# Kernel optimization log

Hardware: AMD Instinct MI355X
Metric: run time of the kernel (lower is better)

## Reference

```python
import jax, jax.numpy as jnp
import numpy as np

B, S, INP, HID = 64, 2048, 512, 512

def setup_inputs() -> dict:
    key = jax.random.key(0)
    ks = jax.random.split(key, 8)
    inp = jax.random.normal(ks[0], (B, INP), dtype=jnp.float32)
    context = jax.random.normal(ks[1], (B, S, INP), dtype=jnp.float32)
    mask = jax.random.randint(ks[2], (B, S), 0, 2) == 1  # True = masked out
    lim_l = 1.0 / np.sqrt(INP)
    Wl = jax.random.uniform(ks[3], (HID, INP), minval=-lim_l, maxval=lim_l, dtype=jnp.float32)
    bl = jax.random.uniform(ks[4], (HID,), minval=-lim_l, maxval=lim_l, dtype=jnp.float32)
    Wc = jax.random.uniform(ks[5], (HID, INP), minval=-lim_l, maxval=lim_l, dtype=jnp.float32)  # Conv1d k=1 weight squeezed
    bc = jax.random.uniform(ks[6], (HID,), minval=-lim_l, maxval=lim_l, dtype=jnp.float32)
    V = jax.random.uniform(ks[7], (HID,), minval=-1.0, maxval=1.0, dtype=jnp.float32)
    return {"inp": inp, "context": context, "mask": mask,
            "Wl": Wl, "bl": bl, "Wc": Wc, "bc": bc, "V": V}

def reference(inp, context, mask, Wl, bl, Wc, bc, V):
    # hid: [B, HID], broadcast over S
    hid = inp @ Wl.T + bl
    # 1x1 Conv1d over permuted context == per-position linear: [B, HID, S]
    ctx = jnp.einsum('bsi,hi->bhs', context, Wc) + bc[None, :, None]
    # additive attention scores: [B, S]
    att = jnp.einsum('h,bhs->bs', V, jnp.tanh(hid[:, :, None] + ctx))
    att = jnp.where(mask, -jnp.inf, att)
    alpha = jax.nn.softmax(att, axis=1)
    # context vector: [B, HID]
    hidden_state = jnp.einsum('bhs,bs->bh', ctx, alpha)
    return (hidden_state, alpha)
```

## Files before the change

### kernel.cpp

```cpp
#include <hip/hip_runtime.h>
#include <hip/hip_bf16.h>
#include <cstdint>
#include <cstddef>

#define B_   64
#define S_   2048
#define INP_ 512
#define HID_ 512

typedef float          floatx4  __attribute__((ext_vector_type(4)));
typedef __bf16         bf16x8   __attribute__((ext_vector_type(8)));
typedef unsigned short ushortx8 __attribute__((ext_vector_type(8)));
typedef unsigned short ushortx4 __attribute__((ext_vector_type(4)));

__device__ __forceinline__ unsigned short f2bf(float f) {
  unsigned u = __float_as_uint(f);
  u += 0x7FFFu + ((u >> 16) & 1u);
  return (unsigned short)(u >> 16);
}
__device__ __forceinline__ float bf2f(unsigned short h) {
  return __uint_as_float(((unsigned)h) << 16);
}
__device__ __forceinline__ float fast_tanh(float x) {
  float u = __builtin_amdgcn_exp2f(x * 2.88539008177792681472f);
  return 1.0f - 2.0f * __builtin_amdgcn_rcpf(u + 1.0f);
}

__global__ void hid_kernel(const float* __restrict__ inp, const float* __restrict__ Wl,
                           const float* __restrict__ bl, float* __restrict__ hid)
{
  __shared__ float ism[512];
  const int b = blockIdx.x, t = threadIdx.x;
  ism[t]       = inp[b * 512 + t];
  ism[t + 256] = inp[b * 512 + 256 + t];
  __syncthreads();
  #pragma unroll
  for (int hh = 0; hh < 2; ++hh) {
    int h = t + hh * 256;
    const float4* wr = (const float4*)(Wl + (size_t)h * 512);
    float4 sv = {0.f, 0.f, 0.f, 0.f};
    for (int i = 0; i < 128; ++i) {
      float4 wv = wr[i];
      float4 iv = *(const float4*)(&ism[i * 4]);
      sv.x += wv.x * iv.x; sv.y += wv.y * iv.y;
      sv.z += wv.z * iv.z; sv.w += wv.w * iv.w;
    }
    hid[b * 512 + h] = bl[h] + sv.x + sv.y + sv.z + sv.w;
  }
}

__global__ void pack_wc_kernel(const float* __restrict__ Wc, unsigned short* __restrict__ pk)
{
  int g = blockIdx.x * 256 + threadIdx.x;
  int l = g & 63, ks = (g >> 6) & 15, m16 = g >> 10;
  int row = m16 * 16 + (l & 15);
  int kb  = ks * 32 + (l >> 4) * 8;
  const float4* s = (const float4*)(Wc + (size_t)row * 512 + kb);
  float4 a = s[0], c = s[1];
  ushortx8 o = { f2bf(a.x), f2bf(a.y), f2bf(a.z), f2bf(a.w),
                 f2bf(c.x), f2bf(c.y), f2bf(c.z), f2bf(c.w) };
  *(ushortx8*)(pk + (size_t)g * 8) = o;
}

template<int MODE>
__global__ __launch_bounds__(256, 2) void ctx_gemm_kernel(
    const float* __restrict__ context, const unsigned short* __restrict__ Wc_pk,
    const float* __restrict__ hid, const float* __restrict__ bc,
    const float* __restrict__ V,
    unsigned short* __restrict__ ctx_out, float* __restrict__ att,
    const float* __restrict__ alpha, float* __restrict__ hidden)
{
  __shared__ alignas(16) unsigned short bsm[64 * 128];
  __shared__ float hid_sm[512];
  __shared__ float V_sm[512];
  __shared__ float bc_sm[512];
  __shared__ float att_sm[64];
  __shared__ float alpha_sm[64];

  const int b    = blockIdx.y;
  const int s0   = blockIdx.x * 64;
  const int t    = threadIdx.x;
  const int lane = t & 63;
  const int w    = t >> 6;
  const int quad = lane >> 4;
  const int l15  = lane & 15;

  for (int i = t; i < 512; i += 256) {
    hid_sm[i] = hid[b * 512 + i];
    V_sm[i]   = V[i];
    bc_sm[i]  = bc[i];
  }
  if (t < 64) {
    att_sm[t] = 0.0f;
    if (MODE == 2) alpha_sm[t] = alpha[b * S_ + s0 + t];
  }

  floatx4 acc[8][4];
  #pragma unroll
  for (int m = 0; m < 8; ++m)
    #pragma unroll
    for (int n = 0; n < 4; ++n) { floatx4 z = {0.f,0.f,0.f,0.f}; acc[m][n] = z; }

  const unsigned short* apBase = Wc_pk + (size_t)(w * 8) * 8192 + lane * 8;
  const float* src = context + ((size_t)b * S_ + s0) * INP_;

  for (int phase = 0; phase < 4; ++phase) {
    __syncthreads();
    #pragma unroll
    for (int i = 0; i < 8; ++i) {
      int id  = t + i * 256;
      int row = id >> 5;
      int c4  = id & 31;
      float4 f = *(const float4*)(src + (size_t)row * INP_ + phase * 128 + c4 * 4);
      int chunk = c4 >> 1, half = c4 & 1;
      int sw = chunk ^ (row & 7);
      ushortx4 hv = { f2bf(f.x), f2bf(f.y), f2bf(f.z), f2bf(f.w) };
      *(ushortx4*)(&bsm[row * 128 + sw * 8 + half * 4]) = hv;
    }
    __syncthreads();
    #pragma unroll
    for (int ksl = 0; ksl < 4; ++ksl) {
      const int ksg = phase * 4 + ksl;
      bf16x8 af[8];
      #pragma unroll
      for (int m = 0; m < 8; ++m)
        af[m] = *(const bf16x8*)(apBase + (size_t)m * 8192 + ksg * 512);
      bf16x8 bfr[4];
      #pragma unroll
      for (int n = 0; n < 4; ++n) {
        int row = n * 16 + l15;
        int c   = ksl * 4 + quad;
        bfr[n] = *(const bf16x8*)(&bsm[row * 128 + ((c ^ (row & 7)) * 8)]);
      }
      #pragma unroll
      for (int m = 0; m < 8; ++m)
        #pragma unroll
        for (int n = 0; n < 4; ++n)
          acc[m][n] = __builtin_amdgcn_mfma_f32_16x16x32_bf16(af[m], bfr[n], acc[m][n], 0, 0, 0);
    }
  }

  if (MODE == 0 || MODE == 1) {
    float attacc[4] = {0.f, 0.f, 0.f, 0.f};
    #pragma unroll
    for (int m = 0; m < 8; ++m) {
      int hb = w * 128 + m * 16 + quad * 4;
      #pragma unroll
      for (int r = 0; r < 4; ++r) {
        int h = hb + r;
        float bcv = bc_sm[h], hv = hid_sm[h], vv = V_sm[h];
        #pragma unroll
        for (int n = 0; n < 4; ++n) {
          float val = acc[m][n][r] + bcv;
          if (MODE == 0)
            ctx_out[((size_t)b * HID_ + h) * S_ + s0 + n * 16 + l15] = f2bf(val);
          attacc[n] += vv * fast_tanh(hv + val);
        }
      }
    }
    #pragma unroll
    for (int n = 0; n < 4; ++n) {
      float v = attacc[n];
      v += __shfl_xor(v, 16);
      v += __shfl_xor(v, 32);
      if (lane < 16) atomicAdd(&att_sm[n * 16 + l15], v);
    }
    __syncthreads();
    if (t < 64) att[b * S_ + s0 + t] = att_sm[t];
  } else {
    #pragma unroll
    for (int m = 0; m < 8; ++m) {
      int hb = w * 128 + m * 16 + quad * 4;
      #pragma unroll
      for (int r = 0; r < 4; ++r) {
        int h = hb + r;
        float bcv = bc_sm[h];
        float hacc = 0.0f;
        #pragma unroll
        for (int n = 0; n < 4; ++n)
          hacc += (acc[m][n][r] + bcv) * alpha_sm[n * 16 + l15];
        hacc += __shfl_xor(hacc, 1);
        hacc += __shfl_xor(hacc, 2);
        hacc += __shfl_xor(hacc, 4);
        hacc += __shfl_xor(hacc, 8);
        if (l15 == 0) atomicAdd(&hidden[b * HID_ + h], hacc);
      }
    }
  }
}

__global__ void softmax_kernel(const void* __restrict__ mask,
                               const float* __restrict__ att,
                               float* __restrict__ alpha)
{
  __shared__ int flags;
  __shared__ float red[8];
  const int b = blockIdx.x, t = threadIdx.x;
  const int lane = t & 63, w = t >> 6;
  if (t == 0) flags = 0;
  __syncthreads();
  int f = 0;
  const unsigned* mw = (const unsigned*)mask;
  for (int i = t; i < 512; i += 256) {
    unsigned v = mw[i];
    if (v > 1u) f |= 1;
    if (v != 0u && v != 0x3f800000u) f |= 2;
  }
  if (f) atomicOr(&flags, f);
  __syncthreads();
  const int fl = flags;
  const int mode = ((fl & 1) == 0) ? 0 : (((fl & 2) == 0) ? 1 : 2);

  float v[8]; bool msk[8];
  float vmax = -1e30f;
  #pragma unroll
  for (int i = 0; i < 8; ++i) {
    int idx = i * 256 + t;
    bool m;
    if (mode == 0)      m = ((const int*)mask)[b * S_ + idx] != 0;
    else if (mode == 1) m = ((const float*)mask)[b * S_ + idx] != 0.0f;
    else                m = ((const unsigned char*)mask)[b * S_ + idx] != 0;
    msk[i] = m;
    v[i] = att[b * S_ + idx];
    if (!m) vmax = fmaxf(vmax, v[i]);
  }
  #pragma unroll
  for (int off = 32; off; off >>= 1) vmax = fmaxf(vmax, __shfl_xor(vmax, off));
  if (lane == 0) red[w] = vmax;
  __syncthreads();
  vmax = fmaxf(fmaxf(red[0], red[1]), fmaxf(red[2], red[3]));

  float e[8], s = 0.0f;
  #pragma unroll
  for (int i = 0; i < 8; ++i) {
    e[i] = msk[i] ? 0.0f : __builtin_amdgcn_exp2f((v[i] - vmax) * 1.4426950408889634f);
    s += e[i];
  }
  #pragma unroll
  for (int off = 32; off; off >>= 1) s += __shfl_xor(s, off);
  if (lane == 0) red[4 + w] = s;
  __syncthreads();
  s = red[4] + red[5] + red[6] + red[7];
  float rinv = 1.0f / s;
  #pragma unroll
  for (int i = 0; i < 8; ++i)
    alpha[b * S_ + i * 256 + t] = e[i] * rinv;
}

__global__ void hidden_kernel(const unsigned short* __restrict__ ctx,
                              const float* __restrict__ alpha,
                              float* __restrict__ hidden)
{
  const int b = blockIdx.y;
  const int w = threadIdx.x >> 6, lane = threadIdx.x & 63;
  const int h = blockIdx.x * 4 + w;
  const unsigned short* cp = ctx + ((size_t)b * HID_ + h) * S_;
  const float* ap = alpha + (size_t)b * S_;
  float acc = 0.0f;
  #pragma unroll
  for (int it = 0; it < 4; ++it) {
    int s = it * 512 + lane * 8;
    ushortx8 cv = *(const ushortx8*)(cp + s);
    float4 a0 = *(const float4*)(ap + s);
    float4 a1 = *(const float4*)(ap + s + 4);
    acc += bf2f(cv[0]) * a0.x + bf2f(cv[1]) * a0.y + bf2f(cv[2]) * a0.z + bf2f(cv[3]) * a0.w
         + bf2f(cv[4]) * a1.x + bf2f(cv[5]) * a1.y + bf2f(cv[6]) * a1.z + bf2f(cv[7]) * a1.w;
  }
  #pragma unroll
  for (int off = 32; off; off >>= 1) acc += __shfl_xor(acc, off);
  if (lane == 0) hidden[b * HID_ + h] = acc;
}

extern "C" void kernel_launch(void* const* d_in, const int* in_sizes, int n_in,
                              void* d_out, int out_size, void* d_ws, size_t ws_size,
                              hipStream_t stream)
{
  const float* inp     = (const float*)d_in[0];
  const float* context = (const float*)d_in[1];
  const void*  mask    = d_in[2];
  const float* Wl      = (const float*)d_in[3];
  const float* bl      = (const float*)d_in[4];
  const float* Wc      = (const float*)d_in[5];
  const float* bc      = (const float*)d_in[6];
  const float* V       = (const float*)d_in[7];

  float* hidden = (float*)d_out;
  float* alpha  = (float*)d_out + B_ * HID_;

  char* ws = (char*)d_ws;
  const size_t CTX_BYTES = (size_t)B_ * HID_ * S_ * 2;
  const size_t HIDW_BYTES = (size_t)B_ * HID_ * 4;
  const size_t ATT_BYTES  = (size_t)B_ * S_ * 4;
  const size_t PK_BYTES   = (size_t)HID_ * INP_ * 2;
  const bool big = ws_size >= CTX_BYTES + HIDW_BYTES + ATT_BYTES + PK_BYTES;

  if (big) {
    unsigned short* ctx_bf = (unsigned short*)ws;
    float* hid_ws          = (float*)(ws + CTX_BYTES);
    float* att_ws          = (float*)(ws + CTX_BYTES + HIDW_BYTES);
    unsigned short* pk     = (unsigned short*)(ws + CTX_BYTES + HIDW_BYTES + ATT_BYTES);

    hid_kernel<<<B_, 256, 0, stream>>>(inp, Wl, bl, hid_ws);
    pack_wc_kernel<<<128, 256, 0, stream>>>(Wc, pk);
    ctx_gemm_kernel<0><<<dim3(S_ / 64, B_), 256, 0, stream>>>(
        context, pk, hid_ws, bc, V, ctx_bf, att_ws, nullptr, nullptr);
    softmax_kernel<<<B_, 256, 0, stream>>>(mask, att_ws, alpha);
    hidden_kernel<<<dim3(HID_ / 4, B_), 256, 0, stream>>>(ctx_bf, alpha, hidden);
  } else {
    float* hid_ws      = (float*)ws;
    float* att_ws      = (float*)(ws + HIDW_BYTES);
    unsigned short* pk = (unsigned short*)(ws + HIDW_BYTES + ATT_BYTES);

    hid_kernel<<<B_, 256, 0, stream>>>(inp, Wl, bl, hid_ws);
    pack_wc_kernel<<<128, 256, 0, stream>>>(Wc, pk);
    ctx_gemm_kernel<1><<<dim3(S_ / 64, B_), 256, 0, stream>>>(
        context, pk, hid_ws, bc, V, nullptr, att_ws, nullptr, nullptr);
    softmax_kernel<<<B_, 256, 0, stream>>>(mask, att_ws, alpha);
    hipMemsetAsync(hidden, 0, HIDW_BYTES, stream);
    ctx_gemm_kernel<2><<<dim3(S_ / 64, B_), 256, 0, stream>>>(
        context, pk, hid_ws, bc, V, nullptr, nullptr, alpha, hidden);
  }
}
```

Measured before the change: 519.9 us.

## Compute hidden state as Wc·(alpha-weighted context) instead of storing ctx

Uses linearity: since alpha sums to one, hidden = Wc·(Σ alpha·context) + bc. The bf16 ctx tensor is no longer written or read back. A new ctxbar kernel reduces context by alpha and a row-GEMV applies Wc and bc. The main GEMM now loads context into LDS with global_load_lds and converts fp32 to bf16 when building the MFMA fragments; hid and V are read from global in the epilogue. This costs a second full read of the fp32 context in exchange for dropping the large ctx write and read; the hid GEMV is also rewritten as a wave-per-row dot product.

```diff
diff --git a/kernel.cpp b/kernel.cpp
--- a/kernel.cpp
+++ b/kernel.cpp
@@ -11,42 +11,31 @@
 typedef float          floatx4  __attribute__((ext_vector_type(4)));
 typedef __bf16         bf16x8   __attribute__((ext_vector_type(8)));
 typedef unsigned short ushortx8 __attribute__((ext_vector_type(8)));
-typedef unsigned short ushortx4 __attribute__((ext_vector_type(4)));
 
 __device__ __forceinline__ unsigned short f2bf(float f) {
   unsigned u = __float_as_uint(f);
   u += 0x7FFFu + ((u >> 16) & 1u);
   return (unsigned short)(u >> 16);
 }
-__device__ __forceinline__ float bf2f(unsigned short h) {
-  return __uint_as_float(((unsigned)h) << 16);
-}
 __device__ __forceinline__ float fast_tanh(float x) {
   float u = __builtin_amdgcn_exp2f(x * 2.88539008177792681472f);
   return 1.0f - 2.0f * __builtin_amdgcn_rcpf(u + 1.0f);
 }
 
-__global__ void hid_kernel(const float* __restrict__ inp, const float* __restrict__ Wl,
-                           const float* __restrict__ bl, float* __restrict__ hid)
-{
-  __shared__ float ism[512];
-  const int b = blockIdx.x, t = threadIdx.x;
-  ism[t]       = inp[b * 512 + t];
-  ism[t + 256] = inp[b * 512 + 256 + t];
-  __syncthreads();
-  #pragma unroll
-  for (int hh = 0; hh < 2; ++hh) {
-    int h = t + hh * 256;
-    const float4* wr = (const float4*)(Wl + (size_t)h * 512);
-    float4 sv = {0.f, 0.f, 0.f, 0.f};
-    for (int i = 0; i < 128; ++i) {
-      float4 wv = wr[i];
-      float4 iv = *(const float4*)(&ism[i * 4]);
-      sv.x += wv.x * iv.x; sv.y += wv.y * iv.y;
-      sv.z += wv.z * iv.z; sv.w += wv.w * iv.w;
-    }
-    hid[b * 512 + h] = bl[h] + sv.x + sv.y + sv.z + sv.w;
-  }
+__global__ void rowgemm_kernel(const float* __restrict__ X, const float* __restrict__ W,
+                               const float* __restrict__ bias, float* __restrict__ out)
+{
+  const int b = blockIdx.y;
+  const int w = threadIdx.x >> 6, lane = threadIdx.x & 63;
+  const int h = blockIdx.x * 4 + w;
+  const float4* wr = (const float4*)(W + (size_t)h * 512) + lane * 2;
+  const float4* xr = (const float4*)(X + (size_t)b * 512) + lane * 2;
+  float4 w0 = wr[0], w1 = wr[1], x0 = xr[0], x1 = xr[1];
+  float acc = w0.x*x0.x + w0.y*x0.y + w0.z*x0.z + w0.w*x0.w
+            + w1.x*x1.x + w1.y*x1.y + w1.z*x1.z + w1.w*x1.w;
+  #pragma unroll
+  for (int off = 32; off; off >>= 1) acc += __shfl_xor(acc, off);
+  if (lane == 0) out[b * 512 + h] = bias[h] + acc;
 }
 
 __global__ void pack_wc_kernel(const float* __restrict__ Wc, unsigned short* __restrict__ pk)
@@ -62,20 +51,12 @@
   *(ushortx8*)(pk + (size_t)g * 8) = o;
 }
 
-template<int MODE>
 __global__ __launch_bounds__(256, 2) void ctx_gemm_kernel(
     const float* __restrict__ context, const unsigned short* __restrict__ Wc_pk,
     const float* __restrict__ hid, const float* __restrict__ bc,
-    const float* __restrict__ V,
-    unsigned short* __restrict__ ctx_out, float* __restrict__ att,
-    const float* __restrict__ alpha, float* __restrict__ hidden)
-{
-  __shared__ alignas(16) unsigned short bsm[64 * 128];
-  __shared__ float hid_sm[512];
-  __shared__ float V_sm[512];
-  __shared__ float bc_sm[512];
-  __shared__ float att_sm[64];
-  __shared__ float alpha_sm[64];
+    const float* __restrict__ V, float* __restrict__ att)
+{
+  __shared__ alignas(16) float tile[64 * 256];
 
   const int b    = blockIdx.y;
   const int s0   = blockIdx.x * 64;
@@ -85,16 +66,6 @@
   const int quad = lane >> 4;
   const int l15  = lane & 15;
 
-  for (int i = t; i < 512; i += 256) {
-    hid_sm[i] = hid[b * 512 + i];
-    V_sm[i]   = V[i];
-    bc_sm[i]  = bc[i];
-  }
-  if (t < 64) {
-    att_sm[t] = 0.0f;
-    if (MODE == 2) alpha_sm[t] = alpha[b * S_ + s0 + t];
-  }
-
   floatx4 acc[8][4];
   #pragma unroll
   for (int m = 0; m < 8; ++m)
@@ -103,24 +74,25 @@
 
   const unsigned short* apBase = Wc_pk + (size_t)(w * 8) * 8192 + lane * 8;
   const float* src = context + ((size_t)b * S_ + s0) * INP_;
-
-  for (int phase = 0; phase < 4; ++phase) {
+  auto* ldsT = (__attribute__((address_space(3))) float*)tile;
+  auto* gsrc = (const __attribute__((address_space(1))) float*)src;
+
+  for (int stage = 0; stage < 2; ++stage) {
     __syncthreads();
     #pragma unroll
-    for (int i = 0; i < 8; ++i) {
+    for (int i = 0; i < 16; ++i) {
       int id  = t + i * 256;
-      int row = id >> 5;
-      int c4  = id & 31;
-      float4 f = *(const float4*)(src + (size_t)row * INP_ + phase * 128 + c4 * 4);
-      int chunk = c4 >> 1, half = c4 & 1;
-      int sw = chunk ^ (row & 7);
-      ushortx4 hv = { f2bf(f.x), f2bf(f.y), f2bf(f.z), f2bf(f.w) };
-      *(ushortx4*)(&bsm[row * 128 + sw * 8 + half * 4]) = hv;
+      int row = id >> 6;
+      int cl  = id & 63;
+      int cg  = cl ^ (row & 7);
+      __builtin_amdgcn_global_load_lds(
+          (const __attribute__((address_space(1))) void*)(gsrc + (size_t)row * INP_ + stage * 256 + cg * 4),
+          (__attribute__((address_space(3))) void*)(ldsT + id * 4), 16, 0, 0);
     }
     __syncthreads();
     #pragma unroll
-    for (int ksl = 0; ksl < 4; ++ksl) {
-      const int ksg = phase * 4 + ksl;
+    for (int ksl = 0; ksl < 8; ++ksl) {
+      const int ksg = stage * 8 + ksl;
       bf16x8 af[8];
       #pragma unroll
       for (int m = 0; m < 8; ++m)
@@ -128,9 +100,16 @@
       bf16x8 bfr[4];
       #pragma unroll
       for (int n = 0; n < 4; ++n) {
-        int row = n * 16 + l15;
-        int c   = ksl * 4 + quad;
-        bfr[n] = *(const bf16x8*)(&bsm[row * 128 + ((c ^ (row & 7)) * 8)]);
+        const int row = n * 16 + l15;
+        const int rw  = row & 7;
+        const int c0  = ksl * 8 + quad * 2;
+        const float4* tp = (const float4*)tile + row * 64;
+        float4 x0 = tp[c0 ^ rw];
+        float4 x1 = tp[(c0 + 1) ^ rw];
+        union { ushortx8 u; bf16x8 h; } cv;
+        cv.u = (ushortx8){ f2bf(x0.x), f2bf(x0.y), f2bf(x0.z), f2bf(x0.w),
+                           f2bf(x1.x), f2bf(x1.y), f2bf(x1.z), f2bf(x1.w) };
+        bfr[n] = cv.h;
       }
       #pragma unroll
       for (int m = 0; m < 8; ++m)
@@ -140,53 +119,32 @@
     }
   }
 
-  if (MODE == 0 || MODE == 1) {
-    float attacc[4] = {0.f, 0.f, 0.f, 0.f};
-    #pragma unroll
-    for (int m = 0; m < 8; ++m) {
-      int hb = w * 128 + m * 16 + quad * 4;
-      #pragma unroll
-      for (int r = 0; r < 4; ++r) {
-        int h = hb + r;
-        float bcv = bc_sm[h], hv = hid_sm[h], vv = V_sm[h];
-        #pragma unroll
-        for (int n = 0; n < 4; ++n) {
-          float val = acc[m][n][r] + bcv;
-          if (MODE == 0)
-            ctx_out[((size_t)b * HID_ + h) * S_ + s0 + n * 16 + l15] = f2bf(val);
-          attacc[n] += vv * fast_tanh(hv + val);
-        }
-      }
-    }
-    #pragma unroll
-    for (int n = 0; n < 4; ++n) {
-      float v = attacc[n];
-      v += __shfl_xor(v, 16);
-      v += __shfl_xor(v, 32);
-      if (lane < 16) atomicAdd(&att_sm[n * 16 + l15], v);
-    }
-    __syncthreads();
-    if (t < 64) att[b * S_ + s0 + t] = att_sm[t];
-  } else {
-    #pragma unroll
-    for (int m = 0; m < 8; ++m) {
-      int hb = w * 128 + m * 16 + quad * 4;
-      #pragma unroll
-      for (int r = 0; r < 4; ++r) {
-        int h = hb + r;
-        float bcv = bc_sm[h];
-        float hacc = 0.0f;
-        #pragma unroll
-        for (int n = 0; n < 4; ++n)
-          hacc += (acc[m][n][r] + bcv) * alpha_sm[n * 16 + l15];
-        hacc += __shfl_xor(hacc, 1);
-        hacc += __shfl_xor(hacc, 2);
-        hacc += __shfl_xor(hacc, 4);
-        hacc += __shfl_xor(hacc, 8);
-        if (l15 == 0) atomicAdd(&hidden[b * HID_ + h], hacc);
-      }
-    }
-  }
+  __syncthreads();
+  if (t < 64) tile[t] = 0.0f;
+  __syncthreads();
+
+  float attacc[4] = {0.f, 0.f, 0.f, 0.f};
+  #pragma unroll
+  for (int m = 0; m < 8; ++m) {
+    const int hb = w * 128 + m * 16 + quad * 4;
+    #pragma unroll
+    for (int r = 0; r < 4; ++r) {
+      const int h = hb + r;
+      const float bcv = bc[h], hv = hid[b * 512 + h], vv = V[h];
+      #pragma unroll
+      for (int n = 0; n < 4; ++n)
+        attacc[n] += vv * fast_tanh(hv + bcv + acc[m][n][r]);
+    }
+  }
+  #pragma unroll
+  for (int n = 0; n < 4; ++n) {
+    float v = attacc[n];
+    v += __shfl_xor(v, 16);
+    v += __shfl_xor(v, 32);
+    if (lane < 16) atomicAdd(&tile[n * 16 + l15], v);
+  }
+  __syncthreads();
+  if (t < 64) att[b * S_ + s0 + t] = tile[t];
 }
 
 __global__ void softmax_kernel(const void* __restrict__ mask,
@@ -247,28 +205,41 @@
     alpha[b * S_ + i * 256 + t] = e[i] * rinv;
 }
 
-__global__ void hidden_kernel(const unsigned short* __restrict__ ctx,
+__global__ void ctxbar_kernel(const float* __restrict__ context,
                               const float* __restrict__ alpha,
-                              float* __restrict__ hidden)
-{
-  const int b = blockIdx.y;
-  const int w = threadIdx.x >> 6, lane = threadIdx.x & 63;
-  const int h = blockIdx.x * 4 + w;
-  const unsigned short* cp = ctx + ((size_t)b * HID_ + h) * S_;
+                              float* __restrict__ ctxbar)
+{
+  __shared__ float4 red[16][16];
+  __shared__ float asm_[S_];
+  const int b = blockIdx.y, i0 = blockIdx.x * 64;
+  const int t = threadIdx.x, i4 = t & 15, sg = t >> 4;
+
   const float* ap = alpha + (size_t)b * S_;
-  float acc = 0.0f;
-  #pragma unroll
-  for (int it = 0; it < 4; ++it) {
-    int s = it * 512 + lane * 8;
-    ushortx8 cv = *(const ushortx8*)(cp + s);
-    float4 a0 = *(const float4*)(ap + s);
-    float4 a1 = *(const float4*)(ap + s + 4);
-    acc += bf2f(cv[0]) * a0.x + bf2f(cv[1]) * a0.y + bf2f(cv[2]) * a0.z + bf2f(cv[3]) * a0.w
-         + bf2f(cv[4]) * a1.x + bf2f(cv[5]) * a1.y + bf2f(cv[6]) * a1.z + bf2f(cv[7]) * a1.w;
-  }
-  #pragma unroll
-  for (int off = 32; off; off >>= 1) acc += __shfl_xor(acc, off);
-  if (lane == 0) hidden[b * HID_ + h] = acc;
+  for (int i = t; i < S_; i += 256) asm_[i] = ap[i];
+  __syncthreads();
+
+  const float* src = context + (size_t)b * S_ * INP_ + i0 + i4 * 4;
+  float4 acc = {0.f, 0.f, 0.f, 0.f};
+  #pragma unroll 4
+  for (int s = sg; s < S_; s += 16) {
+    float wgt = asm_[s];
+    float4 v = *(const float4*)(src + (size_t)s * INP_);
+    acc.x += wgt * v.x; acc.y += wgt * v.y;
+    acc.z += wgt * v.z; acc.w += wgt * v.w;
+  }
+  red[sg][i4] = acc;
+  __syncthreads();
+  #pragma unroll
+  for (int off = 8; off >= 1; off >>= 1) {
+    if (sg < off) {
+      float4 o = red[sg + off][i4];
+      acc.x += o.x; acc.y += o.y; acc.z += o.z; acc.w += o.w;
+      red[sg][i4] = acc;
+    }
+    __syncthreads();
+  }
+  if (sg == 0)
+    *(float4*)(ctxbar + (size_t)b * 512 + i0 + i4 * 4) = acc;
 }
 
 extern "C" void kernel_launch(void* const* d_in, const int* in_sizes, int n_in,
@@ -288,36 +259,15 @@
   float* alpha  = (float*)d_out + B_ * HID_;
 
   char* ws = (char*)d_ws;
-  const size_t CTX_BYTES = (size_t)B_ * HID_ * S_ * 2;
-  const size_t HIDW_BYTES = (size_t)B_ * HID_ * 4;
-  const size_t ATT_BYTES  = (size_t)B_ * S_ * 4;
-  const size_t PK_BYTES   = (size_t)HID_ * INP_ * 2;
-  const bool big = ws_size >= CTX_BYTES + HIDW_BYTES + ATT_BYTES + PK_BYTES;
-
-  if (big) {
-    unsigned short* ctx_bf = (unsigned short*)ws;
-    float* hid_ws          = (float*)(ws + CTX_BYTES);
-    float* att_ws          = (float*)(ws + CTX_BYTES + HIDW_BYTES);
-    unsigned short* pk     = (unsigned short*)(ws + CTX_BYTES + HIDW_BYTES + ATT_BYTES);
-
-    hid_kernel<<<B_, 256, 0, stream>>>(inp, Wl, bl, hid_ws);
-    pack_wc_kernel<<<128, 256, 0, stream>>>(Wc, pk);
-    ctx_gemm_kernel<0><<<dim3(S_ / 64, B_), 256, 0, stream>>>(
-        context, pk, hid_ws, bc, V, ctx_bf, att_ws, nullptr, nullptr);
-    softmax_kernel<<<B_, 256, 0, stream>>>(mask, att_ws, alpha);
-    hidden_kernel<<<dim3(HID_ / 4, B_), 256, 0, stream>>>(ctx_bf, alpha, hidden);
-  } else {
-    float* hid_ws      = (float*)ws;
-    float* att_ws      = (float*)(ws + HIDW_BYTES);
-    unsigned short* pk = (unsigned short*)(ws + HIDW_BYTES + ATT_BYTES);
-
-    hid_kernel<<<B_, 256, 0, stream>>>(inp, Wl, bl, hid_ws);
-    pack_wc_kernel<<<128, 256, 0, stream>>>(Wc, pk);
-    ctx_gemm_kernel<1><<<dim3(S_ / 64, B_), 256, 0, stream>>>(
-        context, pk, hid_ws, bc, V, nullptr, att_ws, nullptr, nullptr);
-    softmax_kernel<<<B_, 256, 0, stream>>>(mask, att_ws, alpha);
-    hipMemsetAsync(hidden, 0, HIDW_BYTES, stream);
-    ctx_gemm_kernel<2><<<dim3(S_ / 64, B_), 256, 0, stream>>>(
-        context, pk, hid_ws, bc, V, nullptr, nullptr, alpha, hidden);
-  }
-}
+  float* hid_ws          = (float*)ws;
+  float* att_ws          = (float*)(ws + (128 << 10));
+  float* ctxbar_ws       = (float*)(ws + (640 << 10));
+  unsigned short* pk     = (unsigned short*)(ws + (768 << 10));
+
+  rowgemm_kernel<<<dim3(HID_ / 4, B_), 256, 0, stream>>>(inp, Wl, bl, hid_ws);
+  pack_wc_kernel<<<128, 256, 0, stream>>>(Wc, pk);
+  ctx_gemm_kernel<<<dim3(S_ / 64, B_), 256, 0, stream>>>(context, pk, hid_ws, bc, V, att_ws);
+  softmax_kernel<<<B_, 256, 0, stream>>>(mask, att_ws, alpha);
+  ctxbar_kernel<<<dim3(8, B_), 256, 0, stream>>>(context, alpha, ctxbar_ws);
+  rowgemm_kernel<<<dim3(HID_ / 4, B_), 256, 0, stream>>>(ctxbar_ws, Wc, bc, hidden);
+}
```

New measurement: 639.5 us. 1.23x slower.
